# Performance work log

Hardware: AMD Instinct MI355X
Metric: run time of the kernel (lower is better)

Reference implementation:

```python
import jax, jax.numpy as jnp
import numpy as np

T, B, E, H, HID, SIG = 1024, 4, 1024, 16, 1024, 64


def setup_inputs() -> dict:
    key = jax.random.key(0)
    ks = jax.random.split(key, 16)
    sc = 0.02
    return {
        "x": jax.random.normal(ks[0], (T, B, E), jnp.float32),
        "Wq": jax.random.normal(ks[1], (E, E), jnp.float32) * sc,
        "bq": jnp.zeros((E,), jnp.float32),
        "Wk": jax.random.normal(ks[2], (E, E), jnp.float32) * sc,
        "bk": jnp.zeros((E,), jnp.float32),
        "Wv": jax.random.normal(ks[3], (E, E), jnp.float32) * sc,
        "bv": jnp.zeros((E,), jnp.float32),
        "Wo": jax.random.normal(ks[4], (E, E), jnp.float32) * sc,
        "bo": jnp.zeros((E,), jnp.float32),
        "W1": jax.random.normal(ks[5], (HID, E), jnp.float32) * sc,
        "b1": jnp.zeros((HID,), jnp.float32),
        "W2": jax.random.normal(ks[6], (SIG, HID), jnp.float32) * sc,
        "b2": jnp.zeros((SIG,), jnp.float32),
        "head_signatures": jax.random.normal(ks[7], (H, SIG), jnp.float32),
    }


def reference(x, Wq, bq, Wk, bk, Wv, bv, Wo, bo, W1, b1, W2, b2, head_signatures):
    # x: (T, B, E) fairseq layout; self-attention, no mask, eval mode (no dropout)
    T_, B_, E_ = x.shape
    H_ = head_signatures.shape[0]
    d = E_ // H_
    scaling = d ** -0.5

    q = (x @ Wq.T + bq) * scaling            # (T,B,E)
    k = x @ Wk.T + bk
    v = x @ Wv.T + bv

    def split_heads(z):                        # (T,B,E) -> (B,H,T,d)
        return z.reshape(T_, B_, H_, d).transpose(1, 2, 0, 3)

    qh, kh, vh = split_heads(q), split_heads(k), split_heads(v)

    scores = jnp.einsum("bhtd,bhsd->bhts", qh, kh)   # (B,H,T,T)
    attn = jax.nn.softmax(scores, axis=-1)
    o = jnp.einsum("bhts,bhsd->bhtd", attn, vh)      # (B,H,T,d)

    # head-competition gate: signature MLP on x, match against head signatures,
    # softmax over heads ('softmax' competition type)
    t = jax.nn.relu(x @ W1.T + b1) @ W2.T + b2       # (T,B,SIG)
    logits = t @ head_signatures.T                   # (T,B,H)
    gate = jax.nn.softmax(logits, axis=-1)
    gate = gate.transpose(1, 2, 0)                   # (B,H,T)

    o = o * gate[..., None]                          # gate per-head outputs
    out = o.transpose(2, 0, 1, 3).reshape(T_, B_, E_)  # (T,B,E)
    return out @ Wo.T + bo
```

## Files before the change

kernel.cpp:

```cpp
#include <hip/hip_runtime.h>

#define Tn   1024
#define Bn   4
#define En   1024
#define Hn   16
#define HIDn 1024
#define SIGn 64
#define Mn   (Tn * Bn)

typedef short  s8x8  __attribute__((ext_vector_type(8)));
typedef float  f32x4 __attribute__((ext_vector_type(4)));

__device__ __forceinline__ unsigned short f2bf(float f) {
    unsigned int x = __float_as_uint(f);
    unsigned int r = (x + 0x7fffu + ((x >> 16) & 1u)) >> 16;
    return (unsigned short)r;
}
__device__ __forceinline__ float exp2asm(float x) {
    float r;
    asm("v_exp_f32 %0, %1" : "=v"(r) : "v"(x));
    return r;
}
__device__ __forceinline__ unsigned int cvtpk(float a, float b) {
    unsigned int r;
    asm("v_cvt_pk_bf16_f32 %0, %1, %2" : "=v"(r) : "v"(a), "v"(b));
    return r;
}

__device__ __forceinline__ void gload_lds16(const void* g, void* l) {
    __builtin_amdgcn_global_load_lds(
        (const __attribute__((address_space(1))) unsigned int*)g,
        (__attribute__((address_space(3))) unsigned int*)l, 16, 0, 0);
}

__device__ __forceinline__ void cast8(const float* s, unsigned short* d) {
    const float4* p = (const float4*)s;
    float4 a = p[0], b = p[1];
    s8x8 o;
    o[0] = (short)f2bf(a.x); o[1] = (short)f2bf(a.y);
    o[2] = (short)f2bf(a.z); o[3] = (short)f2bf(a.w);
    o[4] = (short)f2bf(b.x); o[5] = (short)f2bf(b.y);
    o[6] = (short)f2bf(b.z); o[7] = (short)f2bf(b.w);
    *(s8x8*)d = o;
}

__global__ __launch_bounds__(256) void prep_all(
    const float* __restrict__ x,  const float* __restrict__ W1,
    const float* __restrict__ Wq, const float* __restrict__ Wk,
    const float* __restrict__ Wv, const float* __restrict__ W2,
    const float* __restrict__ b1, const float* __restrict__ bq,
    const float* __restrict__ bk, const float* __restrict__ bv,
    unsigned short* __restrict__ Wcat, unsigned short* __restrict__ W2b,
    float* __restrict__ bcat, unsigned short* __restrict__ xb, int pre)
{
    const size_t WELEM = (size_t)En * En;
    const int y = blockIdx.y, bx = blockIdx.x, tid = threadIdx.x;
    if (y < 4) {
        const float* src = (y == 0) ? W1 : (y == 1) ? Wq : (y == 2) ? Wk : Wv;
        size_t i = (size_t)bx * 256 + tid;
        cast8(src + i * 8, Wcat + y * WELEM + i * 8);
    } else if (y == 4) {
        if (bx < 32) {
            size_t i = (size_t)bx * 256 + tid;
            cast8(W2 + i * 8, W2b + i * 8);
        } else if (bx < 48) {
            int idx = (bx - 32) * 256 + tid;
            int w = idx >> 10;
            const float* s = (w == 0) ? b1 : (w == 1) ? bq : (w == 2) ? bk : bv;
            bcat[idx] = s[idx & 1023];
        }
    } else {
        if (!pre) return;
        int q = y - 5;
        size_t i = (size_t)bx * 256 + tid;
        cast8(x + q * WELEM + i * 8, xb + q * WELEM + i * 8);
    }
}

__global__ __launch_bounds__(512) void fused_proj8(
    const unsigned short* __restrict__ Xb,
    const unsigned short* __restrict__ Wcat, const float* __restrict__ bcat,
    unsigned short* __restrict__ t1b, unsigned short* __restrict__ qb,
    unsigned short* __restrict__ kb, unsigned short* __restrict__ vb)
{
    __shared__ __align__(16) short As[2][256 * 64];
    __shared__ __align__(16) short Bs[2][256 * 64];

    const int tid  = threadIdx.x;
    const int w    = tid >> 6;
    const int lane = tid & 63;
    const int ln15 = lane & 15;
    const int kq   = lane >> 4;
    const int wr   = w >> 2;
    const int wc   = w & 3;
    const int bn   = blockIdx.x;
    const int bm   = blockIdx.y;
    const size_t rowA0 = (size_t)bm * 256;
    const size_t rowB0 = (size_t)bn * 256;

    const int rl = lane >> 3;
    const int cg = (lane & 7) ^ rl;
    const unsigned short* Abase = Xb   + (rowA0 + w * 8 + rl) * 1024 + cg * 8;
    const unsigned short* Bbase = Wcat + (rowB0 + w * 8 + rl) * 1024 + cg * 8;
    const int ldsW = w * 512;

    f32x4 acc[8][4];
#pragma unroll
    for (int m = 0; m < 8; m++)
#pragma unroll
        for (int n = 0; n < 4; n++) acc[m][n] = (f32x4){0.f, 0.f, 0.f, 0.f};

    auto STG = [&](int buf, int k0) {
#pragma unroll
        for (int i = 0; i < 4; i++)
            gload_lds16(Abase + (size_t)i * 64 * 1024 + k0,
                        &As[buf][i * 4096 + ldsW]);
#pragma unroll
        for (int i = 0; i < 4; i++)
            gload_lds16(Bbase + (size_t)i * 64 * 1024 + k0,
                        &Bs[buf][i * 4096 + ldsW]);
    };

    auto COMPUTE = [&](const short* lA, const short* lB) {
#pragma unroll
        for (int q = 0; q < 4; q++) {
            const int rh = q >> 1, ch = q & 1;
            s8x8 af[4][2], bf[2][2];
#pragma unroll
            for (int m = 0; m < 2 + 2; m++) {
                int row = wr * 128 + (rh * 4 + m) * 16 + ln15;
#pragma unroll
                for (int kk = 0; kk < 2; kk++)
                    af[m][kk] = *(const s8x8*)&lA[row * 64 +
                        (((kk * 4 + kq) ^ (row & 7)) * 8)];
            }
#pragma unroll
            for (int n = 0; n < 2; n++) {
                int row = wc * 64 + (ch * 2 + n) * 16 + ln15;
#pragma unroll
                for (int kk = 0; kk < 2; kk++)
                    bf[n][kk] = *(const s8x8*)&lB[row * 64 +
                        (((kk * 4 + kq) ^ (row & 7)) * 8)];
            }
            __builtin_amdgcn_s_setprio(1);
#pragma unroll
            for (int m = 0; m < 4; m++)
#pragma unroll
                for (int n = 0; n < 2; n++)
#pragma unroll
                    for (int kk = 0; kk < 2; kk++)
                        acc[rh * 4 + m][ch * 2 + n] =
                            __builtin_amdgcn_mfma_f32_16x16x32_bf16(
                                af[m][kk], bf[n][kk],
                                acc[rh * 4 + m][ch * 2 + n], 0, 0, 0);
            __builtin_amdgcn_s_setprio(0);
        }
    };

    STG(0, 0);
    STG(1, 64);

    for (int t = 0; t < 16; t++) {
        if (t < 15)
            asm volatile("s_waitcnt vmcnt(8)" ::: "memory");
        else
            asm volatile("s_waitcnt vmcnt(0)" ::: "memory");
        __builtin_amdgcn_s_barrier();
        asm volatile("" ::: "memory");
        COMPUTE(&As[t & 1][0], &Bs[t & 1][0]);
        asm volatile("" ::: "memory");
        __builtin_amdgcn_s_barrier();
        if (t + 2 < 16) STG(t & 1, (t + 2) * 64);
    }

    const int which = bn >> 2;
    unsigned short* dst = (which == 0) ? t1b : (which == 1) ? qb
                        : (which == 2) ? kb : vb;
    const float scale = (which == 1) ? 0.18033688011112042f : 1.0f;
    const int   relu  = (which == 0);
    const int   cbase = (bn & 3) * 256;

    float bcol[4];
#pragma unroll
    for (int n = 0; n < 4; n++)
        bcol[n] = bcat[bn * 256 + wc * 64 + n * 16 + ln15];
#pragma unroll
    for (int m = 0; m < 8; m++) {
        size_t gr0 = rowA0 + wr * 128 + m * 16 + kq * 4;
#pragma unroll
        for (int n = 0; n < 4; n++) {
            int gc = cbase + wc * 64 + n * 16 + ln15;
#pragma unroll
            for (int j = 0; j < 4; j++) {
                float vv = acc[m][n][j] + bcol[n];
                if (relu) vv = fmaxf(vv, 0.f);
                vv *= scale;
                dst[(gr0 + j) * 1024 + gc] = f2bf(vv);
            }
        }
    }
}

__global__ __launch_bounds__(256) void fused_proj_fb(
    const float* __restrict__ X,
    const unsigned short* __restrict__ Wcat, const float* __restrict__ bcat,
    unsigned short* __restrict__ t1b, unsigned short* __restrict__ qb,
    unsigned short* __restrict__ kb, unsigned short* __restrict__ vb)
{
    __shared__ __align__(16) short As[128 * 32];
    __shared__ __align__(16) short Bs[128 * 32];
    const int tid  = threadIdx.x;
    const int wave = tid >> 6;
    const int lane = tid & 63;
    const int ln15 = lane & 15;
    const int kq   = lane >> 4;
    const int wr   = wave >> 1;
    const int wc   = wave & 1;
    const int bn   = blockIdx.x;
    const int bm   = blockIdx.y;
    const size_t rowA0 = (size_t)bm * 128;
    const size_t rowB0 = (size_t)bn * 128;
    const int lrow   = lane >> 2;
    const int lchunk = lane & 3;

    f32x4 acc[4][4];
#pragma unroll
    for (int m = 0; m < 4; m++)
#pragma unroll
        for (int n = 0; n < 4; n++) acc[m][n] = (f32x4){0.f, 0.f, 0.f, 0.f};

    for (int k0 = 0; k0 < 1024; k0 += 32) {
#pragma unroll
        for (int i = 0; i < 2; i++) {
            int row = wave * 32 + i * 16 + lrow;
            int c   = lchunk ^ ((row >> 1) & 3);
            gload_lds16(Wcat + (rowB0 + row) * 1024 + k0 + c * 8,
                        &Bs[(wave * 32 + i * 16) * 32]);
        }
        {
            const int srow = tid >> 1;
            const int scol = (tid & 1) * 16;
            const float4* src = (const float4*)(X + (rowA0 + srow) * 1024 + k0 + scol);
            float4 a = src[0], b = src[1], c4 = src[2], d4 = src[3];
            s8x8 v0, v1;
            v0[0] = (short)f2bf(a.x);  v0[1] = (short)f2bf(a.y);
            v0[2] = (short)f2bf(a.z);  v0[3] = (short)f2bf(a.w);
            v0[4] = (short)f2bf(b.x);  v0[5] = (short)f2bf(b.y);
            v0[6] = (short)f2bf(b.z);  v0[7] = (short)f2bf(b.w);
            v1[0] = (short)f2bf(c4.x); v1[1] = (short)f2bf(c4.y);
            v1[2] = (short)f2bf(c4.z); v1[3] = (short)f2bf(c4.w);
            v1[4] = (short)f2bf(d4.x); v1[5] = (short)f2bf(d4.y);
            v1[6] = (short)f2bf(d4.z); v1[7] = (short)f2bf(d4.w);
            int sw = (srow >> 1) & 3;
            int c0 = (scol >> 3) ^ sw;
            int c1 = ((scol >> 3) + 1) ^ sw;
            *(s8x8*)&As[srow * 32 + c0 * 8] = v0;
            *(s8x8*)&As[srow * 32 + c1 * 8] = v1;
        }
        asm volatile("s_waitcnt vmcnt(0)" ::: "memory");
        __syncthreads();

        s8x8 af[4], bf[4];
#pragma unroll
        for (int m = 0; m < 4; m++) {
            int row = wr * 64 + m * 16 + ln15;
            af[m] = *(const s8x8*)&As[row * 32 + (kq ^ ((row >> 1) & 3)) * 8];
        }
#pragma unroll
        for (int n = 0; n < 4; n++) {
            int row = wc * 64 + n * 16 + ln15;
            bf[n] = *(const s8x8*)&Bs[row * 32 + (kq ^ ((row >> 1) & 3)) * 8];
        }
#pragma unroll
        for (int m = 0; m < 4; m++)
#pragma unroll
            for (int n = 0; n < 4; n++)
                acc[m][n] = __builtin_amdgcn_mfma_f32_16x16x32_bf16(
                    af[m], bf[n], acc[m][n], 0, 0, 0);
        __syncthreads();
    }

    const int which = bn >> 3;
    unsigned short* dst = (which == 0) ? t1b : (which == 1) ? qb
                        : (which == 2) ? kb : vb;
    const float scale = (which == 1) ? 0.18033688011112042f : 1.0f;
    const int   relu  = (which == 0);
    const int   cbase = (bn & 7) * 128;

    float bcol[4];
#pragma unroll
    for (int n = 0; n < 4; n++)
        bcol[n] = bcat[bn * 128 + wc * 64 + n * 16 + ln15];
#pragma unroll
    for (int m = 0; m < 4; m++) {
        size_t gr0 = rowA0 + wr * 64 + m * 16 + kq * 4;
#pragma unroll
        for (int n = 0; n < 4; n++) {
            int gc = cbase + wc * 64 + n * 16 + ln15;
#pragma unroll
            for (int j = 0; j < 4; j++) {
                float vv = acc[m][n][j] + bcol[n];
                if (relu) vv = fmaxf(vv, 0.f);
                vv *= scale;
                dst[(gr0 + j) * 1024 + gc] = f2bf(vv);
            }
        }
    }
}

__global__ __launch_bounds__(256) void out_proj(
    const unsigned short* __restrict__ A, const unsigned short* __restrict__ W,
    const float* __restrict__ bias, float* __restrict__ C)
{
    __shared__ __align__(16) short As[64 * 32];
    __shared__ __align__(16) short Bs[128 * 32];
    const int tid  = threadIdx.x;
    const int wave = tid >> 6;
    const int lane = tid & 63;
    const int ln15 = lane & 15;
    const int kq   = lane >> 4;
    const int wr   = wave >> 1;
    const int wc   = wave & 1;
    const size_t rowA0 = (size_t)blockIdx.y * 64;
    const size_t rowB0 = (size_t)blockIdx.x * 128;
    const int lrow   = lane >> 2;
    const int lchunk = lane & 3;

    f32x4 acc[2][4];
#pragma unroll
    for (int m = 0; m < 2; m++)
#pragma unroll
        for (int n = 0; n < 4; n++) acc[m][n] = (f32x4){0.f, 0.f, 0.f, 0.f};

    for (int k0 = 0; k0 < 1024; k0 += 32) {
        {
            int row = wave * 16 + lrow;
            int c   = lchunk ^ ((row >> 1) & 3);
            gload_lds16(A + (rowA0 + row) * 1024 + k0 + c * 8,
                        &As[(wave * 16) * 32]);
        }
#pragma unroll
        for (int i = 0; i < 2; i++) {
            int row = wave * 32 + i * 16 + lrow;
            int c   = lchunk ^ ((row >> 1) & 3);
            gload_lds16(W + (rowB0 + row) * 1024 + k0 + c * 8,
                        &Bs[(wave * 32 + i * 16) * 32]);
        }
        asm volatile("s_waitcnt vmcnt(0)" ::: "memory");
        __syncthreads();

        s8x8 af[2], bf[4];
#pragma unroll
        for (int m = 0; m < 2; m++) {
            int row = wr * 32 + m * 16 + ln15;
            af[m] = *(const s8x8*)&As[row * 32 + (kq ^ ((row >> 1) & 3)) * 8];
        }
#pragma unroll
        for (int n = 0; n < 4; n++) {
            int row = wc * 64 + n * 16 + ln15;
            bf[n] = *(const s8x8*)&Bs[row * 32 + (kq ^ ((row >> 1) & 3)) * 8];
        }
#pragma unroll
        for (int m = 0; m < 2; m++)
#pragma unroll
            for (int n = 0; n < 4; n++)
                acc[m][n] = __builtin_amdgcn_mfma_f32_16x16x32_bf16(
                    af[m], bf[n], acc[m][n], 0, 0, 0);
        __syncthreads();
    }

    float bcol[4];
#pragma unroll
    for (int n = 0; n < 4; n++)
        bcol[n] = bias[rowB0 + wc * 64 + n * 16 + ln15];
#pragma unroll
    for (int m = 0; m < 2; m++) {
        size_t gr0 = rowA0 + wr * 32 + m * 16 + kq * 4;
#pragma unroll
        for (int n = 0; n < 4; n++) {
            size_t gc = rowB0 + wc * 64 + n * 16 + ln15;
#pragma unroll
            for (int j = 0; j < 4; j++)
                C[(gr0 + j) * 1024 + gc] = acc[m][n][j] + bcol[n];
        }
    }
}

__device__ __forceinline__ void t2gate_body(
    int blk, int tid,
    const unsigned short* __restrict__ t1, const unsigned short* __restrict__ W2b,
    const float* __restrict__ b2, const float* __restrict__ hs,
    float* __restrict__ gate,
    short* As, short* Bs, float (*t2s)[65], float (*hss)[65])
{
    const int wave  = tid >> 6;
    const int lane  = tid & 63;
    const int ln15  = lane & 15;
    const int kq    = lane >> 4;
    const int lrow8 = lane >> 3;
    const int lch   = lane & 7;
    const int m0    = blk * 16;

    {
        int r = tid >> 4, c = (tid & 15) * 4;
        float4 v = *(const float4*)(hs + r * 64 + c);
        hss[r][c] = v.x; hss[r][c + 1] = v.y; hss[r][c + 2] = v.z; hss[r][c + 3] = v.w;
    }

    f32x4 acc = (f32x4){0.f, 0.f, 0.f, 0.f};
    for (int k0 = 0; k0 < 1024; k0 += 64) {
        if (wave < 2) {
            int row = wave * 8 + lrow8;
            int cg  = lch ^ (row & 7);
            gload_lds16(t1 + (size_t)(m0 + row) * 1024 + k0 + cg * 8,
                        As + (wave * 8) * 64);
        }
#pragma unroll
        for (int i = 0; i < 2; i++) {
            int row = wave * 16 + i * 8 + lrow8;
            int cg  = lch ^ (row & 7);
            gload_lds16(W2b + (size_t)row * 1024 + k0 + cg * 8,
                        Bs + (wave * 16 + i * 8) * 64);
        }
        asm volatile("s_waitcnt vmcnt(0)" ::: "memory");
        __syncthreads();

#pragma unroll
        for (int kk = 0; kk < 2; kk++) {
            int arow = ln15;
            int brow = wave * 16 + ln15;
            s8x8 af = *(const s8x8*)(As + arow * 64 + (((kk * 4 + kq) ^ (arow & 7)) * 8));
            s8x8 bf = *(const s8x8*)(Bs + brow * 64 + (((kk * 4 + kq) ^ (brow & 7)) * 8));
            acc = __builtin_amdgcn_mfma_f32_16x16x32_bf16(af, bf, acc, 0, 0, 0);
        }
        __syncthreads();
    }

#pragma unroll
    for (int j = 0; j < 4; j++)
        t2s[kq * 4 + j][wave * 16 + ln15] = acc[j] + b2[wave * 16 + ln15];
    __syncthreads();

    int r = tid >> 4, hd = tid & 15;
    float s = 0.f;
#pragma unroll 16
    for (int d = 0; d < 64; d++) s += t2s[r][d] * hss[hd][d];
    float mx = s;
    mx = fmaxf(mx, __shfl_xor(mx, 1));
    mx = fmaxf(mx, __shfl_xor(mx, 2));
    mx = fmaxf(mx, __shfl_xor(mx, 4));
    mx = fmaxf(mx, __shfl_xor(mx, 8));
    float e = __expf(s - mx);
    float sum = e;
    sum += __shfl_xor(sum, 1);
    sum += __shfl_xor(sum, 2);
    sum += __shfl_xor(sum, 4);
    sum += __shfl_xor(sum, 8);
    gate[(size_t)(m0 + r) * Hn + hd] = e / sum;
}

__device__ __forceinline__ void vtrans_body(
    int bh, int t0, int tid,
    const unsigned short* __restrict__ vb, unsigned short* __restrict__ vt,
    unsigned short (*ts)[65])
{
    const int b = bh >> 4, h = bh & 15;
    {
        int tr = tid >> 2, dq = (tid & 3) * 16;
        const unsigned short* src =
            vb + ((size_t)(t0 + tr) * Bn + b) * En + h * 64 + dq;
        s8x8 a = *(const s8x8*)src;
        s8x8 c = *(const s8x8*)(src + 8);
#pragma unroll
        for (int i = 0; i < 8; i++) {
            ts[tr][dq + i]     = (unsigned short)a[i];
            ts[tr][dq + 8 + i] = (unsigned short)c[i];
        }
    }
    __syncthreads();
    {
        int dr = tid >> 2, tq = (tid & 3) * 16;
        unsigned short* dst = vt + ((size_t)bh * 64 + dr) * Tn + t0 + tq;
        s8x8 o0, o1;
#pragma unroll
        for (int i = 0; i < 8; i++) {
            o0[i] = (short)ts[tq + i][dr];
            o1[i] = (short)ts[tq + 8 + i][dr];
        }
        *(s8x8*)dst = o0;
        *(s8x8*)(dst + 8) = o1;
    }
}

__global__ __launch_bounds__(256) void t2gate_k(
    const unsigned short* __restrict__ t1, const unsigned short* __restrict__ W2b,
    const float* __restrict__ b2, const float* __restrict__ hs,
    float* __restrict__ gate)
{
    __shared__ __align__(16) short As[16 * 64];
    __shared__ __align__(16) short Bs[64 * 64];
    __shared__ float t2s[16][65];
    __shared__ float hss[16][65];
    t2gate_body(blockIdx.x, threadIdx.x, t1, W2b, b2, hs, gate, As, Bs, t2s, hss);
}
__global__ __launch_bounds__(256) void trans_wo_k(
    const unsigned short* __restrict__ vb, unsigned short* __restrict__ vt,
    const float* __restrict__ Wo, unsigned short* __restrict__ Wob)
{
    const int bx = blockIdx.x, tid = threadIdx.x;
    if (bx >= 1024) {
        size_t i = (size_t)(bx - 1024) * 256 + tid;
        cast8(Wo + i * 8, Wob + i * 8);
        return;
    }
    __shared__ unsigned short ts[64][65];
    vtrans_body(bx & 63, (bx >> 6) * 64, tid, vb, vt, ts);
}

__global__ __launch_bounds__(256) void midstage(
    const unsigned short* __restrict__ t1, const unsigned short* __restrict__ W2b,
    const float* __restrict__ b2, const float* __restrict__ hs,
    float* __restrict__ gate,
    const unsigned short* __restrict__ vb, unsigned short* __restrict__ vt,
    const float* __restrict__ Wo, unsigned short* __restrict__ Wob)
{
    __shared__ __align__(16) short As[16 * 64];
    __shared__ __align__(16) short Bs[64 * 64];
    __shared__ float t2s[16][65];
    __shared__ float hss[16][65];
    __shared__ unsigned short ts[64][65];
    const int bx = blockIdx.x, tid = threadIdx.x;
    if (bx < 256) {
        t2gate_body(bx, tid, t1, W2b, b2, hs, gate, As, Bs, t2s, hss);
    } else if (bx < 1280) {
        int v = bx - 256;
        vtrans_body(v & 63, (v >> 6) * 64, tid, vb, vt, ts);
    } else {
        size_t i = (size_t)(bx - 1280) * 256 + tid;
        cast8(Wo + i * 8, Wob + i * 8);
    }
}

__global__ __launch_bounds__(512, 2) void attn_mfma(
    const unsigned short* __restrict__ q, const unsigned short* __restrict__ k,
    const unsigned short* __restrict__ vt, const float* __restrict__ gate,
    unsigned short* __restrict__ o)
{
    __shared__ __align__(16) short Kls[2][64 * 64];
    __shared__ __align__(16) short Vls[2][64 * 64];

    const int tid  = threadIdx.x;
    const int w    = tid >> 6;
    const int lane = tid & 63;
    const int ln   = lane & 15;
    const int kq   = lane >> 4;
    const int bh   = blockIdx.x;
    const int b    = bh >> 4;
    const int h    = bh & 15;
    const int qt   = blockIdx.y;

    s8x8 qf[2];
    {
        const int qrow = qt * 128 + w * 16 + ln;
        const unsigned short* src =
            q + ((size_t)qrow * Bn + b) * En + h * 64 + kq * 8;
        qf[0] = *(const s8x8*)(src);
        qf[1] = *(const s8x8*)(src + 32);
    }

    f32x4 OT[4];
#pragma unroll
    for (int n = 0; n < 4; n++) OT[n] = (f32x4){0.f, 0.f, 0.f, 0.f};
    float mrun = -1e30f, lrun = 0.f;

    const int srow = w * 8 + (lane >> 3);
    const int sch  = (lane & 7) ^ (srow & 7);
    const int sn  = srow >> 4;
    const int sK0 = 32 * (sn >> 1) + 4 * (sn & 1)
                  + 8 * ((srow >> 2) & 3) + (srow & 3);

    auto stage = [&](int bufi, int s0) {
        const unsigned short* gk =
            k + ((size_t)(s0 + sK0) * Bn + b) * En + h * 64 + sch * 8;
        gload_lds16(gk, &Kls[bufi][w * 512]);
        const unsigned short* gv =
            vt + ((size_t)bh * 64 + srow) * Tn + s0 + sch * 8;
        gload_lds16(gv, &Vls[bufi][w * 512]);
    };

    stage(0, 0);
    asm volatile("s_waitcnt vmcnt(0)" ::: "memory");
    __syncthreads();

    int cur = 0;
    for (int t = 0; t < Tn / 64; t++) {
        if (t + 1 < Tn / 64) stage(cur ^ 1, (t + 1) * 64);

        f32x4 S[4];
        __builtin_amdgcn_s_setprio(1);
#pragma unroll
        for (int n = 0; n < 4; n++) {
            S[n] = (f32x4){0.f, 0.f, 0.f, 0.f};
#pragma unroll
            for (int kk = 0; kk < 2; kk++) {
                int row = n * 16 + ln;
                int cc  = (kk * 4 + kq) ^ (row & 7);
                s8x8 kf = *(const s8x8*)&Kls[cur][row * 64 + cc * 8];
                S[n] = __builtin_amdgcn_mfma_f32_16x16x32_bf16(kf, qf[kk], S[n], 0, 0, 0);
            }
        }
        __builtin_amdgcn_s_setprio(0);

        float rm;
        {
            f32x4 t0 = S[0];
#pragma unroll
            for (int n = 1; n < 4; n++) {
                t0[0] = fmaxf(t0[0], S[n][0]); t0[1] = fmaxf(t0[1], S[n][1]);
                t0[2] = fmaxf(t0[2], S[n][2]); t0[3] = fmaxf(t0[3], S[n][3]);
            }
            rm = fmaxf(fmaxf(t0[0], t0[1]), fmaxf(t0[2], t0[3]));
            rm = fmaxf(rm, __shfl_xor(rm, 16));
            rm = fmaxf(rm, __shfl_xor(rm, 32));
        }

        if (__any(rm > mrun + 8.0f)) {
            float mnew = fmaxf(mrun, rm);
            float fs = exp2asm(mrun - mnew);
            lrun *= fs;
#pragma unroll
            for (int n = 0; n < 4; n++) {
                OT[n][0] *= fs; OT[n][1] *= fs; OT[n][2] *= fs; OT[n][3] *= fs;
            }
            mrun = mnew;
        }

        float ps = 0.f;
#pragma unroll
        for (int n = 0; n < 4; n++) {
            S[n][0] = exp2asm(S[n][0] - mrun); ps += S[n][0];
            S[n][1] = exp2asm(S[n][1] - mrun); ps += S[n][1];
            S[n][2] = exp2asm(S[n][2] - mrun); ps += S[n][2];
            S[n][3] = exp2asm(S[n][3] - mrun); ps += S[n][3];
        }
        ps += __shfl_xor(ps, 16);
        ps += __shfl_xor(ps, 32);
        lrun += ps;

        union { unsigned int u[4]; s8x8 v; } pb[2];
#pragma unroll
        for (int kk = 0; kk < 2; kk++) {
            pb[kk].u[0] = cvtpk(S[2 * kk][0],     S[2 * kk][1]);
            pb[kk].u[1] = cvtpk(S[2 * kk][2],     S[2 * kk][3]);
            pb[kk].u[2] = cvtpk(S[2 * kk + 1][0], S[2 * kk + 1][1]);
            pb[kk].u[3] = cvtpk(S[2 * kk + 1][2], S[2 * kk + 1][3]);
        }

        __builtin_amdgcn_s_setprio(1);
#pragma unroll
        for (int kk = 0; kk < 2; kk++) {
#pragma unroll
            for (int n = 0; n < 4; n++) {
                int row = n * 16 + ln;
                int cv  = (kk * 4 + kq) ^ (row & 7);
                s8x8 vf = *(const s8x8*)&Vls[cur][row * 64 + cv * 8];
                OT[n] = __builtin_amdgcn_mfma_f32_16x16x32_bf16(vf, pb[kk].v, OT[n], 0, 0, 0);
            }
        }
        __builtin_amdgcn_s_setprio(0);

        asm volatile("s_waitcnt vmcnt(0)" ::: "memory");
        __syncthreads();
        cur ^= 1;
    }

    {
        int tq = qt * 128 + w * 16 + ln;
        size_t m = (size_t)tq * Bn + b;
        float g = gate[m * Hn + h] / lrun;
        unsigned short* dst = o + m * En + h * 64;
#pragma unroll
        for (int n = 0; n < 4; n++) {
            int d0 = n * 16 + kq * 4;
            uint2 pkv;
            pkv.x = cvtpk(OT[n][0] * g, OT[n][1] * g);
            pkv.y = cvtpk(OT[n][2] * g, OT[n][3] * g);
            *(uint2*)(dst + d0) = pkv;
        }
    }
}

extern "C" void kernel_launch(void* const* d_in, const int* in_sizes, int n_in,
                              void* d_out, int out_size, void* d_ws, size_t ws_size,
                              hipStream_t stream)
{
    const float* x  = (const float*)d_in[0];
    const float* Wq = (const float*)d_in[1];
    const float* bq = (const float*)d_in[2];
    const float* Wk = (const float*)d_in[3];
    const float* bk = (const float*)d_in[4];
    const float* Wv = (const float*)d_in[5];
    const float* bv = (const float*)d_in[6];
    const float* Wo = (const float*)d_in[7];
    const float* bo = (const float*)d_in[8];
    const float* W1 = (const float*)d_in[9];
    const float* b1 = (const float*)d_in[10];
    const float* W2 = (const float*)d_in[11];
    const float* b2 = (const float*)d_in[12];
    const float* hs = (const float*)d_in[13];

    const size_t WELEM = (size_t)En * En;
    unsigned short* Wcat = (unsigned short*)d_ws;
    unsigned short* W2b  = Wcat + 4 * WELEM;
    float* bcat = (float*)(W2b + (size_t)SIGn * HIDn);
    float* gate = bcat + 4096;
    unsigned short* t1b = (unsigned short*)(gate + (size_t)Mn * Hn);
    unsigned short* qb  = t1b + (size_t)Mn * En;
    unsigned short* kb  = qb  + (size_t)Mn * En;
    unsigned short* vb  = kb  + (size_t)Mn * En;
    unsigned short* xb  = vb  + (size_t)Mn * En;
    unsigned short* Wob = Wcat;
    unsigned short* ob  = vb;

    const size_t need_xb =
        (size_t)((char*)(xb + (size_t)Mn * En) - (char*)d_ws);
    const bool pre = ws_size >= need_xb;

    dim3 blk(256);

    prep_all<<<dim3(512, 9), blk, 0, stream>>>(
        x, W1, Wq, Wk, Wv, W2, b1, bq, bk, bv, Wcat, W2b, bcat, xb, (int)pre);

    if (pre) {
        unsigned short* vtb = xb;
        fused_proj8<<<dim3(16, 16), dim3(512), 0, stream>>>(
            xb, Wcat, bcat, t1b, qb, kb, vb);
        midstage<<<dim3(1792), blk, 0, stream>>>(
            t1b, W2b, b2, hs, gate, vb, vtb, Wo, Wob);
        attn_mfma<<<dim3(Bn * Hn, Tn / 128), dim3(512), 0, stream>>>(
            qb, kb, vtb, gate, ob);
    } else {
        unsigned short* vtb = t1b;
        fused_proj_fb<<<dim3(32, 32), blk, 0, stream>>>(
            x, Wcat, bcat, t1b, qb, kb, vb);
        t2gate_k<<<dim3(Mn / 16), blk, 0, stream>>>(t1b, W2b, b2, hs, gate);
        trans_wo_k<<<dim3(1536), blk, 0, stream>>>(vb, vtb, Wo, Wob);
        attn_mfma<<<dim3(Bn * Hn, Tn / 128), dim3(512), 0, stream>>>(
            qb, kb, vtb, gate, ob);
    }

    out_proj<<<dim3(En / 128, Mn / 64), blk, 0, stream>>>(ob, Wob, bo, (float*)d_out);
}
```

Before: 113.0 us.

## Use triple-buffered BK=32 pipeline with single barrier in fused projection GEMM

```diff
diff --git a/kernel.cpp b/kernel.cpp
--- a/kernel.cpp
+++ b/kernel.cpp
@@ -83,8 +83,8 @@
     unsigned short* __restrict__ t1b, unsigned short* __restrict__ qb,
     unsigned short* __restrict__ kb, unsigned short* __restrict__ vb)
 {
-    __shared__ __align__(16) short As[2][256 * 64];
-    __shared__ __align__(16) short Bs[2][256 * 64];
+    __shared__ __align__(16) short As[3][256 * 32];
+    __shared__ __align__(16) short Bs[3][256 * 32];
 
     const int tid  = threadIdx.x;
     const int w    = tid >> 6;
@@ -98,11 +98,15 @@
     const size_t rowA0 = (size_t)bm * 256;
     const size_t rowB0 = (size_t)bn * 256;
 
-    const int rl = lane >> 3;
-    const int cg = (lane & 7) ^ rl;
-    const unsigned short* Abase = Xb   + (rowA0 + w * 8 + rl) * 1024 + cg * 8;
-    const unsigned short* Bbase = Wcat + (rowB0 + w * 8 + rl) * 1024 + cg * 8;
-    const int ldsW = w * 512;
+    const unsigned short* Pa[2];
+    const unsigned short* Pb[2];
+#pragma unroll
+    for (int i = 0; i < 2; i++) {
+        int r = w * 32 + i * 16 + (lane >> 2);
+        int c = (lane & 3) ^ ((r >> 1) & 3);
+        Pa[i] = Xb   + (rowA0 + r) * 1024 + c * 8;
+        Pb[i] = Wcat + (rowB0 + r) * 1024 + c * 8;
+    }
 
     f32x4 acc[8][4];
 #pragma unroll
@@ -110,67 +114,60 @@
 #pragma unroll
         for (int n = 0; n < 4; n++) acc[m][n] = (f32x4){0.f, 0.f, 0.f, 0.f};
 
-    auto STG = [&](int buf, int k0) {
-#pragma unroll
-        for (int i = 0; i < 4; i++)
-            gload_lds16(Abase + (size_t)i * 64 * 1024 + k0,
-                        &As[buf][i * 4096 + ldsW]);
-#pragma unroll
-        for (int i = 0; i < 4; i++)
-            gload_lds16(Bbase + (size_t)i * 64 * 1024 + k0,
-                        &Bs[buf][i * 4096 + ldsW]);
+    auto STG = [&](int buf, int t) {
+        const int off = t * 32;
+#pragma unroll
+        for (int i = 0; i < 2; i++)
+            gload_lds16(Pa[i] + off, &As[buf][(w * 32 + i * 16) * 32]);
+#pragma unroll
+        for (int i = 0; i < 2; i++)
+            gload_lds16(Pb[i] + off, &Bs[buf][(w * 32 + i * 16) * 32]);
     };
 
-    auto COMPUTE = [&](const short* lA, const short* lB) {
-#pragma unroll
-        for (int q = 0; q < 4; q++) {
-            const int rh = q >> 1, ch = q & 1;
-            s8x8 af[4][2], bf[2][2];
-#pragma unroll
-            for (int m = 0; m < 2 + 2; m++) {
-                int row = wr * 128 + (rh * 4 + m) * 16 + ln15;
-#pragma unroll
-                for (int kk = 0; kk < 2; kk++)
-                    af[m][kk] = *(const s8x8*)&lA[row * 64 +
-                        (((kk * 4 + kq) ^ (row & 7)) * 8)];
-            }
-#pragma unroll
-            for (int n = 0; n < 2; n++) {
-                int row = wc * 64 + (ch * 2 + n) * 16 + ln15;
-#pragma unroll
-                for (int kk = 0; kk < 2; kk++)
-                    bf[n][kk] = *(const s8x8*)&lB[row * 64 +
-                        (((kk * 4 + kq) ^ (row & 7)) * 8)];
+    auto COMPUTE = [&](int buf) {
+        const short* lA = &As[buf][0];
+        const short* lB = &Bs[buf][0];
+        s8x8 bf[4];
+#pragma unroll
+        for (int n = 0; n < 4; n++) {
+            int row = wc * 64 + n * 16 + ln15;
+            bf[n] = *(const s8x8*)&lB[row * 32 + ((kq ^ ((row >> 1) & 3)) * 8)];
+        }
+#pragma unroll
+        for (int rh = 0; rh < 2; rh++) {
+            s8x8 af[4];
+#pragma unroll
+            for (int m = 0; m < 4; m++) {
+                int row = wr * 128 + rh * 64 + m * 16 + ln15;
+                af[m] = *(const s8x8*)&lA[row * 32 + ((kq ^ ((row >> 1) & 3)) * 8)];
             }
             __builtin_amdgcn_s_setprio(1);
 #pragma unroll
             for (int m = 0; m < 4; m++)
 #pragma unroll
-                for (int n = 0; n < 2; n++)
-#pragma unroll
-                    for (int kk = 0; kk < 2; kk++)
-                        acc[rh * 4 + m][ch * 2 + n] =
-                            __builtin_amdgcn_mfma_f32_16x16x32_bf16(
-                                af[m][kk], bf[n][kk],
-                                acc[rh * 4 + m][ch * 2 + n], 0, 0, 0);
+                for (int n = 0; n < 4; n++)
+                    acc[rh * 4 + m][n] = __builtin_amdgcn_mfma_f32_16x16x32_bf16(
+                        af[m], bf[n], acc[rh * 4 + m][n], 0, 0, 0);
             __builtin_amdgcn_s_setprio(0);
         }
     };
 
     STG(0, 0);
-    STG(1, 64);
-
-    for (int t = 0; t < 16; t++) {
-        if (t < 15)
-            asm volatile("s_waitcnt vmcnt(8)" ::: "memory");
+    STG(1, 1);
+
+    int cur = 0, sb = 2;
+    for (int t = 0; t < 32; t++) {
+        if (t < 31)
+            asm volatile("s_waitcnt vmcnt(4)" ::: "memory");
         else
             asm volatile("s_waitcnt vmcnt(0)" ::: "memory");
         __builtin_amdgcn_s_barrier();
         asm volatile("" ::: "memory");
-        COMPUTE(&As[t & 1][0], &Bs[t & 1][0]);
+        if (t + 2 < 32) STG(sb, t + 2);
+        COMPUTE(cur);
         asm volatile("" ::: "memory");
-        __builtin_amdgcn_s_barrier();
-        if (t + 2 < 16) STG(t & 1, (t + 2) * 64);
+        cur = (cur == 2) ? 0 : cur + 1;
+        sb  = (sb == 2) ? 0 : sb + 1;
     }
 
     const int which = bn >> 2;
```

New measurement: 116.3 us. 2.9% more time.
